# Kernel optimization log

Hardware: AMD Instinct MI355X
Metric: run time of the kernel (lower is better)

The kernel has to match this reference:

```python
import jax, jax.numpy as jnp
import numpy as np

B, F, E = 2048, 24, 128
P = F * (F - 1) // 2  # 276 upper-triangular field pairs


def setup_inputs() -> dict:
    key = jax.random.key(0)
    k1, k2 = jax.random.split(key)
    x = jax.random.normal(k1, (B, F, E), dtype=jnp.float32)
    # keras random_normal initializer uses small stddev; 0.05 mirrors that
    kernel = jax.random.normal(k2, (E, P, E), dtype=jnp.float32) * 0.05
    return {"x": x, "kernel": kernel}


def reference(x, kernel):
    F_ = x.shape[1]
    p_idx, q_idx = np.triu_indices(F_, k=1)  # static pair index lists (i < j)
    Xp = x[:, p_idx, :]  # [B, P, E]
    Xq = x[:, q_idx, :]  # [B, P, E]
    # result[b,p] = sum_{d,e} Xp[b,p,e] * kernel[d,p,e] * Xq[b,p,d]
    # fused einsum avoids the [B, E, P, E] intermediate the TF code materializes
    result = jnp.einsum("bpe,dpe,bpd->bp", Xp, kernel, Xq)
    return result
```

## Files before the change

### kernel.cpp

```cpp
#include <hip/hip_runtime.h>
#include <stdint.h>

#define B_SZ 2048
#define F_SZ 24
#define E_SZ 128
#define P_SZ 276
#define NWG  (P_SZ * 8)

#define XT_ELEMS (B_SZ * F_SZ * E_SZ)
#define KB_ELEMS (P_SZ * E_SZ * E_SZ)
#define WS_NEED  ((size_t)(XT_ELEMS + KB_ELEMS) * 2)

#define XPREP_BLKS (F_SZ * 64)
#define KPREP_BLKS (P_SZ * 4)

typedef __bf16 bf16x8 __attribute__((ext_vector_type(8)));
typedef __bf16 bf16x4 __attribute__((ext_vector_type(4)));
typedef float  f32x16 __attribute__((ext_vector_type(16)));

__global__ __launch_bounds__(256) void prepack_all(
    const float* __restrict__ x, const float* __restrict__ kern,
    __bf16* __restrict__ xft, __bf16* __restrict__ kbf)
{
    const int bid = blockIdx.x;
    const int tid = threadIdx.x;
    __shared__ float sT[32][129];
    if (bid < XPREP_BLKS) {
        const int f = bid >> 6, grp = bid & 63;
        {
            const int row = tid >> 3, c0 = (tid & 7) * 16;
            const float* src = x + ((size_t)(grp * 32 + row) * F_SZ + f) * E_SZ + c0;
            float4 v0 = ((const float4*)src)[0];
            float4 v1 = ((const float4*)src)[1];
            float4 v2 = ((const float4*)src)[2];
            float4 v3 = ((const float4*)src)[3];
            *(float4*)&sT[row][c0]      = v0;
            *(float4*)&sT[row][c0 + 4]  = v1;
            *(float4*)&sT[row][c0 + 8]  = v2;
            *(float4*)&sT[row][c0 + 12] = v3;
        }
        __syncthreads();
        __bf16* dst = xft + (size_t)(f * 64 + grp) * 4096;
#pragma unroll
        for (int u = 0; u < 2; ++u) {
            const int s = tid * 2 + u;
            const int row = s & 31;
            const int e0  = (s >> 6) * 16 + ((s >> 5) & 1) * 8;
            bf16x8 h;
#pragma unroll
            for (int i = 0; i < 8; ++i)
                h[i] = (__bf16)sT[row][e0 + i];
            *(bf16x8*)(dst + s * 8) = h;
        }
    } else {
        const int kb = bid - XPREP_BLKS;
        const int p = kb >> 2, mt = kb & 3;
        {
            const int row = tid >> 3, c0 = (tid & 7) * 16;
            const float* src = kern + ((size_t)(mt * 32 + row) * P_SZ + p) * E_SZ + c0;
            float4 v0 = ((const float4*)src)[0];
            float4 v1 = ((const float4*)src)[1];
            float4 v2 = ((const float4*)src)[2];
            float4 v3 = ((const float4*)src)[3];
            *(float4*)&sT[row][c0]      = v0;
            *(float4*)&sT[row][c0 + 4]  = v1;
            *(float4*)&sT[row][c0 + 8]  = v2;
            *(float4*)&sT[row][c0 + 12] = v3;
        }
        __syncthreads();
        __bf16* dst = kbf + (size_t)p * 16384 + mt * 4096;
#pragma unroll
        for (int u = 0; u < 2; ++u) {
            const int s = tid * 2 + u;
            const int lane = s & 63, l31 = lane & 31, hi2 = lane >> 5;
            const int e0 = (s >> 6) * 16 + hi2 * 8;
            bf16x8 h;
#pragma unroll
            for (int i = 0; i < 8; ++i)
                h[i] = (__bf16)sT[l31][e0 + i];
            *(bf16x8*)(dst + s * 8) = h;
        }
    }
}

__global__ __launch_bounds__(512) void opn_main(
    const __bf16* __restrict__ xft, const __bf16* __restrict__ kbf,
    float* __restrict__ out)
{
    const int tid = threadIdx.x, w = tid >> 6, lane = tid & 63;
    const int l31 = lane & 31, hi = lane >> 5;
    const int orig = blockIdx.x;
    const int bb = orig & 7;
    const int p  = orig >> 3;

    int fp = 0, rem = p;
    while (rem >= F_SZ - 1 - fp) { rem -= F_SZ - 1 - fp; ++fp; }
    const int fq = fp + 1 + rem;

    const int grp = bb * 8 + w;

    bf16x8 xpf[8];
    const __bf16* xpb = xft + (size_t)(fp * 64 + grp) * 4096 + lane * 8;
#pragma unroll
    for (int kk = 0; kk < 8; ++kk)
        xpf[kk] = *(const bf16x8*)(xpb + kk * 512);

    bf16x4 xqr[4][4];
    const __bf16* xqb = xft + (size_t)(fq * 64 + grp) * 4096 + l31 * 8 + hi * 4;
#pragma unroll
    for (int mt = 0; mt < 4; ++mt)
#pragma unroll
        for (int q = 0; q < 4; ++q)
            xqr[mt][q] = *(const bf16x4*)(xqb + (mt * 2 + (q >> 1)) * 512 + (q & 1) * 256);

    const __bf16* kpb = kbf + (size_t)p * 16384 + lane * 8;
    float s0 = 0.f, s1 = 0.f;
#pragma unroll
    for (int mt = 0; mt < 4; ++mt) {
        bf16x8 kf[8];
#pragma unroll
        for (int kk = 0; kk < 8; ++kk)
            kf[kk] = *(const bf16x8*)(kpb + (mt * 8 + kk) * 512);
        f32x16 acc;
#pragma unroll
        for (int q = 0; q < 16; ++q) acc[q] = 0.f;
#pragma unroll
        for (int kk = 0; kk < 8; ++kk)
            acc = __builtin_amdgcn_mfma_f32_32x32x16_bf16(kf[kk], xpf[kk], acc, 0, 0, 0);
#pragma unroll
        for (int q = 0; q < 4; ++q) {
            const bf16x4 xq = xqr[mt][q];
            s0 += acc[q * 4 + 0] * (float)xq[0] + acc[q * 4 + 1] * (float)xq[1];
            s1 += acc[q * 4 + 2] * (float)xq[2] + acc[q * 4 + 3] * (float)xq[3];
        }
    }
    float s = s0 + s1;
    s += __shfl_xor(s, 32);
    if (hi == 0)
        out[(size_t)(grp * 32 + l31) * P_SZ + p] = s;
}

__global__ __launch_bounds__(512, 4) void opn_fallback(
    const float* __restrict__ x, const float* __restrict__ kern,
    float* __restrict__ out)
{
    __shared__ short sA[128 * E_SZ];
    __shared__ short sB[E_SZ * E_SZ];
    __shared__ float red[2][128];

    const int tid = threadIdx.x;
    const int orig = blockIdx.x;
    const int nwg2 = P_SZ * 16;
    const int wgid = (orig & 7) * (nwg2 / 8) + (orig >> 3);
    const int p  = wgid >> 4;
    const int bb = wgid & 15;
    const int b0 = bb * 128;

    int fp = 0, rem = p;
    while (rem >= F_SZ - 1 - fp) { rem -= F_SZ - 1 - fp; ++fp; }
    const int fq = fp + 1 + rem;

#pragma unroll
    for (int k = 0; k < 4; ++k) {
        int i = tid + k * 512;
        int r = i >> 4, s8 = i & 15;
        const float* src = x + ((size_t)(b0 + r) * F_SZ + fp) * E_SZ + s8 * 8;
        float4 v0 = *(const float4*)src;
        float4 v1 = *(const float4*)(src + 4);
        bf16x8 h;
        h[0] = (__bf16)v0.x; h[1] = (__bf16)v0.y; h[2] = (__bf16)v0.z; h[3] = (__bf16)v0.w;
        h[4] = (__bf16)v1.x; h[5] = (__bf16)v1.y; h[6] = (__bf16)v1.z; h[7] = (__bf16)v1.w;
        *(bf16x8*)&sA[r * E_SZ + ((s8 ^ (r & 15)) << 3)] = h;
    }
#pragma unroll
    for (int k = 0; k < 4; ++k) {
        int i = tid + k * 512;
        int r = i >> 4, s8 = i & 15;
        const float* src = kern + ((size_t)r * P_SZ + p) * E_SZ + s8 * 8;
        float4 v0 = *(const float4*)src;
        float4 v1 = *(const float4*)(src + 4);
        bf16x8 h;
        h[0] = (__bf16)v0.x; h[1] = (__bf16)v0.y; h[2] = (__bf16)v0.z; h[3] = (__bf16)v0.w;
        h[4] = (__bf16)v1.x; h[5] = (__bf16)v1.y; h[6] = (__bf16)v1.z; h[7] = (__bf16)v1.w;
        *(bf16x8*)&sB[r * E_SZ + ((s8 ^ (r & 15)) << 3)] = h;
    }
    __syncthreads();

    const int w = tid >> 6, lane = tid & 63;
    const int l31 = lane & 31, hi = lane >> 5;
    const int mh = w >> 2, ng = w & 3;

    f32x16 acc[2];
#pragma unroll
    for (int mt = 0; mt < 2; ++mt)
#pragma unroll
        for (int j = 0; j < 16; ++j) acc[mt][j] = 0.f;

    const int brow = ng * 32 + l31;
#pragma unroll
    for (int kk = 0; kk < 8; ++kk) {
        const int e8 = kk * 2 + hi;
        bf16x8 bfr = *(const bf16x8*)&sA[brow * E_SZ + ((e8 ^ (brow & 15)) << 3)];
#pragma unroll
        for (int mt = 0; mt < 2; ++mt) {
            int arow = (mh * 2 + mt) * 32 + l31;
            bf16x8 afr = *(const bf16x8*)&sB[arow * E_SZ + ((e8 ^ (arow & 15)) << 3)];
            acc[mt] = __builtin_amdgcn_mfma_f32_32x32x16_bf16(afr, bfr, acc[mt], 0, 0, 0);
        }
    }

    const float* xqp = x + ((size_t)(b0 + brow) * F_SZ + fq) * E_SZ;
    float sv = 0.f;
#pragma unroll
    for (int mt = 0; mt < 2; ++mt) {
        const int dbase = (mh * 2 + mt) * 32 + hi * 4;
#pragma unroll
        for (int q = 0; q < 4; ++q) {
            float4 xq = *(const float4*)(xqp + dbase + q * 8);
            sv += acc[mt][q * 4 + 0] * xq.x + acc[mt][q * 4 + 1] * xq.y
                + acc[mt][q * 4 + 2] * xq.z + acc[mt][q * 4 + 3] * xq.w;
        }
    }
    sv += __shfl_xor(sv, 32);
    if (hi == 0) red[mh][brow] = sv;
    __syncthreads();

    if (tid < 128)
        out[(size_t)(b0 + tid) * P_SZ + p] = red[0][tid] + red[1][tid];
}

extern "C" void kernel_launch(void* const* d_in, const int* in_sizes, int n_in,
                              void* d_out, int out_size, void* d_ws, size_t ws_size,
                              hipStream_t stream) {
    const float* x    = (const float*)d_in[0];
    const float* kern = (const float*)d_in[1];
    float* out = (float*)d_out;

    if (ws_size >= WS_NEED) {
        __bf16* xft = (__bf16*)d_ws;
        __bf16* kbf = xft + XT_ELEMS;
        prepack_all<<<dim3(XPREP_BLKS + KPREP_BLKS), 256, 0, stream>>>(x, kern, xft, kbf);
        opn_main<<<dim3(NWG), 512, 0, stream>>>(xft, kbf, out);
    } else {
        opn_fallback<<<dim3(P_SZ * 16), 512, 0, stream>>>(x, kern, out);
    }
}
```

Measured before the change: 56.81 us.

## Drop kernel prepack; convert kernel slice into swizzled LDS per pair

```diff
diff --git a/kernel.cpp b/kernel.cpp
--- a/kernel.cpp
+++ b/kernel.cpp
@@ -5,139 +5,132 @@
 #define F_SZ 24
 #define E_SZ 128
 #define P_SZ 276
-#define NWG  (P_SZ * 8)
+#define NWG  552
 
 #define XT_ELEMS (B_SZ * F_SZ * E_SZ)
-#define KB_ELEMS (P_SZ * E_SZ * E_SZ)
-#define WS_NEED  ((size_t)(XT_ELEMS + KB_ELEMS) * 2)
+#define WS_NEED  ((size_t)XT_ELEMS * 2)
 
 #define XPREP_BLKS (F_SZ * 64)
-#define KPREP_BLKS (P_SZ * 4)
 
 typedef __bf16 bf16x8 __attribute__((ext_vector_type(8)));
 typedef __bf16 bf16x4 __attribute__((ext_vector_type(4)));
 typedef float  f32x16 __attribute__((ext_vector_type(16)));
 
-__global__ __launch_bounds__(256) void prepack_all(
-    const float* __restrict__ x, const float* __restrict__ kern,
-    __bf16* __restrict__ xft, __bf16* __restrict__ kbf)
+__global__ __launch_bounds__(256) void prepack_x(
+    const float* __restrict__ x, __bf16* __restrict__ xft)
 {
     const int bid = blockIdx.x;
     const int tid = threadIdx.x;
+    const int f = bid >> 6, grp = bid & 63;
     __shared__ float sT[32][129];
-    if (bid < XPREP_BLKS) {
-        const int f = bid >> 6, grp = bid & 63;
-        {
-            const int row = tid >> 3, c0 = (tid & 7) * 16;
-            const float* src = x + ((size_t)(grp * 32 + row) * F_SZ + f) * E_SZ + c0;
-            float4 v0 = ((const float4*)src)[0];
-            float4 v1 = ((const float4*)src)[1];
-            float4 v2 = ((const float4*)src)[2];
-            float4 v3 = ((const float4*)src)[3];
-            *(float4*)&sT[row][c0]      = v0;
-            *(float4*)&sT[row][c0 + 4]  = v1;
-            *(float4*)&sT[row][c0 + 8]  = v2;
-            *(float4*)&sT[row][c0 + 12] = v3;
-        }
-        __syncthreads();
-        __bf16* dst = xft + (size_t)(f * 64 + grp) * 4096;
-#pragma unroll
-        for (int u = 0; u < 2; ++u) {
-            const int s = tid * 2 + u;
-            const int row = s & 31;
-            const int e0  = (s >> 6) * 16 + ((s >> 5) & 1) * 8;
-            bf16x8 h;
-#pragma unroll
-            for (int i = 0; i < 8; ++i)
-                h[i] = (__bf16)sT[row][e0 + i];
-            *(bf16x8*)(dst + s * 8) = h;
-        }
-    } else {
-        const int kb = bid - XPREP_BLKS;
-        const int p = kb >> 2, mt = kb & 3;
-        {
-            const int row = tid >> 3, c0 = (tid & 7) * 16;
-            const float* src = kern + ((size_t)(mt * 32 + row) * P_SZ + p) * E_SZ + c0;
-            float4 v0 = ((const float4*)src)[0];
-            float4 v1 = ((const float4*)src)[1];
-            float4 v2 = ((const float4*)src)[2];
-            float4 v3 = ((const float4*)src)[3];
-            *(float4*)&sT[row][c0]      = v0;
-            *(float4*)&sT[row][c0 + 4]  = v1;
-            *(float4*)&sT[row][c0 + 8]  = v2;
-            *(float4*)&sT[row][c0 + 12] = v3;
-        }
-        __syncthreads();
-        __bf16* dst = kbf + (size_t)p * 16384 + mt * 4096;
-#pragma unroll
-        for (int u = 0; u < 2; ++u) {
-            const int s = tid * 2 + u;
-            const int lane = s & 63, l31 = lane & 31, hi2 = lane >> 5;
-            const int e0 = (s >> 6) * 16 + hi2 * 8;
-            bf16x8 h;
-#pragma unroll
-            for (int i = 0; i < 8; ++i)
-                h[i] = (__bf16)sT[l31][e0 + i];
-            *(bf16x8*)(dst + s * 8) = h;
-        }
-    }
-}
-
-__global__ __launch_bounds__(512) void opn_main(
-    const __bf16* __restrict__ xft, const __bf16* __restrict__ kbf,
+    {
+        const int row = tid >> 3, c0 = (tid & 7) * 16;
+        const float* src = x + ((size_t)(grp * 32 + row) * F_SZ + f) * E_SZ + c0;
+        float4 v0 = ((const float4*)src)[0];
+        float4 v1 = ((const float4*)src)[1];
+        float4 v2 = ((const float4*)src)[2];
+        float4 v3 = ((const float4*)src)[3];
+        *(float4*)&sT[row][c0]      = v0;
+        *(float4*)&sT[row][c0 + 4]  = v1;
+        *(float4*)&sT[row][c0 + 8]  = v2;
+        *(float4*)&sT[row][c0 + 12] = v3;
+    }
+    __syncthreads();
+    __bf16* dst = xft + (size_t)(f * 64 + grp) * 4096;
+#pragma unroll
+    for (int u = 0; u < 2; ++u) {
+        const int s = tid * 2 + u;
+        const int row = s & 31;
+        const int e0  = (s >> 6) * 16 + ((s >> 5) & 1) * 8;
+        bf16x8 h;
+#pragma unroll
+        for (int i = 0; i < 8; ++i)
+            h[i] = (__bf16)sT[row][e0 + i];
+        *(bf16x8*)(dst + s * 8) = h;
+    }
+}
+
+__global__ __launch_bounds__(512, 4) void opn_main(
+    const __bf16* __restrict__ xft, const float* __restrict__ kern,
     float* __restrict__ out)
 {
+    __shared__ short sK[E_SZ * E_SZ];
+
     const int tid = threadIdx.x, w = tid >> 6, lane = tid & 63;
     const int l31 = lane & 31, hi = lane >> 5;
     const int orig = blockIdx.x;
-    const int bb = orig & 7;
-    const int p  = orig >> 3;
+    const int xcd = orig & 7;
+    const int p = ((xcd >> 1) * 69) + (orig >> 3);
+    const int h = xcd & 1;
 
     int fp = 0, rem = p;
     while (rem >= F_SZ - 1 - fp) { rem -= F_SZ - 1 - fp; ++fp; }
     const int fq = fp + 1 + rem;
 
-    const int grp = bb * 8 + w;
-
-    bf16x8 xpf[8];
-    const __bf16* xpb = xft + (size_t)(fp * 64 + grp) * 4096 + lane * 8;
-#pragma unroll
-    for (int kk = 0; kk < 8; ++kk)
-        xpf[kk] = *(const bf16x8*)(xpb + kk * 512);
-
-    bf16x4 xqr[4][4];
-    const __bf16* xqb = xft + (size_t)(fq * 64 + grp) * 4096 + l31 * 8 + hi * 4;
-#pragma unroll
-    for (int mt = 0; mt < 4; ++mt)
-#pragma unroll
-        for (int q = 0; q < 4; ++q)
-            xqr[mt][q] = *(const bf16x4*)(xqb + (mt * 2 + (q >> 1)) * 512 + (q & 1) * 256);
-
-    const __bf16* kpb = kbf + (size_t)p * 16384 + lane * 8;
-    float s0 = 0.f, s1 = 0.f;
-#pragma unroll
-    for (int mt = 0; mt < 4; ++mt) {
-        bf16x8 kf[8];
+    {
+        const int d = tid >> 2, c = tid & 3;
+        const float* kr = kern + ((size_t)d * P_SZ + p) * E_SZ + c * 32;
+        float4 v[8];
+#pragma unroll
+        for (int j = 0; j < 8; ++j) v[j] = ((const float4*)kr)[j];
+        const int dsw = d & 15;
+#pragma unroll
+        for (int j = 0; j < 4; ++j) {
+            bf16x8 hh;
+            hh[0] = (__bf16)v[2*j].x;   hh[1] = (__bf16)v[2*j].y;
+            hh[2] = (__bf16)v[2*j].z;   hh[3] = (__bf16)v[2*j].w;
+            hh[4] = (__bf16)v[2*j+1].x; hh[5] = (__bf16)v[2*j+1].y;
+            hh[6] = (__bf16)v[2*j+1].z; hh[7] = (__bf16)v[2*j+1].w;
+            const int s = c * 4 + j;
+            *(bf16x8*)&sK[d * E_SZ + ((s ^ dsw) << 3)] = hh;
+        }
+    }
+    __syncthreads();
+
+#pragma unroll
+    for (int t = 0; t < 4; ++t) {
+        const int grp = h * 32 + t * 8 + w;
+
+        bf16x8 xpf[8];
+        const __bf16* xpb = xft + (size_t)(fp * 64 + grp) * 4096 + lane * 8;
 #pragma unroll
         for (int kk = 0; kk < 8; ++kk)
-            kf[kk] = *(const bf16x8*)(kpb + (mt * 8 + kk) * 512);
-        f32x16 acc;
-#pragma unroll
-        for (int q = 0; q < 16; ++q) acc[q] = 0.f;
-#pragma unroll
-        for (int kk = 0; kk < 8; ++kk)
-            acc = __builtin_amdgcn_mfma_f32_32x32x16_bf16(kf[kk], xpf[kk], acc, 0, 0, 0);
-#pragma unroll
-        for (int q = 0; q < 4; ++q) {
-            const bf16x4 xq = xqr[mt][q];
-            s0 += acc[q * 4 + 0] * (float)xq[0] + acc[q * 4 + 1] * (float)xq[1];
-            s1 += acc[q * 4 + 2] * (float)xq[2] + acc[q * 4 + 3] * (float)xq[3];
-        }
-    }
-    float s = s0 + s1;
-    s += __shfl_xor(s, 32);
-    if (hi == 0)
-        out[(size_t)(grp * 32 + l31) * P_SZ + p] = s;
+            xpf[kk] = *(const bf16x8*)(xpb + kk * 512);
+
+        bf16x4 xqr[4][4];
+        const __bf16* xqb = xft + (size_t)(fq * 64 + grp) * 4096 + l31 * 8 + hi * 4;
+#pragma unroll
+        for (int mt = 0; mt < 4; ++mt)
+#pragma unroll
+            for (int q = 0; q < 4; ++q)
+                xqr[mt][q] = *(const bf16x4*)(xqb + (mt * 2 + (q >> 1)) * 512 + (q & 1) * 256);
+
+        float s0 = 0.f, s1 = 0.f;
+#pragma unroll
+        for (int mt = 0; mt < 4; ++mt) {
+            const int arow = mt * 32 + l31;
+            const short* kRow = &sK[arow * E_SZ];
+            const int asw = (arow & 15) << 3;
+            f32x16 acc;
+#pragma unroll
+            for (int q = 0; q < 16; ++q) acc[q] = 0.f;
+#pragma unroll
+            for (int kk = 0; kk < 8; ++kk) {
+                bf16x8 afr = *(const bf16x8*)&kRow[((kk * 2 + hi) << 3) ^ asw];
+                acc = __builtin_amdgcn_mfma_f32_32x32x16_bf16(afr, xpf[kk], acc, 0, 0, 0);
+            }
+#pragma unroll
+            for (int q = 0; q < 4; ++q) {
+                const bf16x4 xq = xqr[mt][q];
+                s0 += acc[q * 4 + 0] * (float)xq[0] + acc[q * 4 + 1] * (float)xq[1];
+                s1 += acc[q * 4 + 2] * (float)xq[2] + acc[q * 4 + 3] * (float)xq[3];
+            }
+        }
+        float s = s0 + s1;
+        s += __shfl_xor(s, 32);
+        if (hi == 0)
+            out[(size_t)(grp * 32 + l31) * P_SZ + p] = s;
+    }
 }
 
 __global__ __launch_bounds__(512, 4) void opn_fallback(
@@ -167,10 +160,10 @@
         const float* src = x + ((size_t)(b0 + r) * F_SZ + fp) * E_SZ + s8 * 8;
         float4 v0 = *(const float4*)src;
         float4 v1 = *(const float4*)(src + 4);
-        bf16x8 h;
-        h[0] = (__bf16)v0.x; h[1] = (__bf16)v0.y; h[2] = (__bf16)v0.z; h[3] = (__bf16)v0.w;
-        h[4] = (__bf16)v1.x; h[5] = (__bf16)v1.y; h[6] = (__bf16)v1.z; h[7] = (__bf16)v1.w;
-        *(bf16x8*)&sA[r * E_SZ + ((s8 ^ (r & 15)) << 3)] = h;
+        bf16x8 hh;
+        hh[0] = (__bf16)v0.x; hh[1] = (__bf16)v0.y; hh[2] = (__bf16)v0.z; hh[3] = (__bf16)v0.w;
+        hh[4] = (__bf16)v1.x; hh[5] = (__bf16)v1.y; hh[6] = (__bf16)v1.z; hh[7] = (__bf16)v1.w;
+        *(bf16x8*)&sA[r * E_SZ + ((s8 ^ (r & 15)) << 3)] = hh;
     }
 #pragma unroll
     for (int k = 0; k < 4; ++k) {
@@ -179,10 +172,10 @@
         const float* src = kern + ((size_t)r * P_SZ + p) * E_SZ + s8 * 8;
         float4 v0 = *(const float4*)src;
         float4 v1 = *(const float4*)(src + 4);
-        bf16x8 h;
-        h[0] = (__bf16)v0.x; h[1] = (__bf16)v0.y; h[2] = (__bf16)v0.z; h[3] = (__bf16)v0.w;
-        h[4] = (__bf16)v1.x; h[5] = (__bf16)v1.y; h[6] = (__bf16)v1.z; h[7] = (__bf16)v1.w;
-        *(bf16x8*)&sB[r * E_SZ + ((s8 ^ (r & 15)) << 3)] = h;
+        bf16x8 hh;
+        hh[0] = (__bf16)v0.x; hh[1] = (__bf16)v0.y; hh[2] = (__bf16)v0.z; hh[3] = (__bf16)v0.w;
+        hh[4] = (__bf16)v1.x; hh[5] = (__bf16)v1.y; hh[6] = (__bf16)v1.z; hh[7] = (__bf16)v1.w;
+        *(bf16x8*)&sB[r * E_SZ + ((s8 ^ (r & 15)) << 3)] = hh;
     }
     __syncthreads();
 
@@ -238,9 +231,8 @@
 
     if (ws_size >= WS_NEED) {
         __bf16* xft = (__bf16*)d_ws;
-        __bf16* kbf = xft + XT_ELEMS;
-        prepack_all<<<dim3(XPREP_BLKS + KPREP_BLKS), 256, 0, stream>>>(x, kern, xft, kbf);
-        opn_main<<<dim3(NWG), 512, 0, stream>>>(xft, kbf, out);
+        prepack_x<<<dim3(XPREP_BLKS), 256, 0, stream>>>(x, xft);
+        opn_main<<<dim3(NWG), 512, 0, stream>>>(xft, kern, out);
     } else {
         opn_fallback<<<dim3(P_SZ * 16), 512, 0, stream>>>(x, kern, out);
     }
```

Measured after the change: 50.30 us. -11.5%, faster.
